# Kernel optimization log

Hardware: AMD Instinct MI355X
Metric: run time of the kernel (lower is better)

Reference implementation:

```python
import jax, jax.numpy as jnp
import numpy as np

NEG_SLOPE = 0.2  # PyG GATv2Conv default


def gatv2_layer(h, src, dst, Wl, bl, Wr, br, att, bias, n):
    # h: [N, din]; src/dst: [E'] (self-loops included)
    xl = h @ Wl + bl                      # [N, d] source-side transform (lin_l)
    xr = h @ Wr + br                      # [N, d] target-side transform (lin_r)
    s = xl[src] + xr[dst]                 # [E', d] per-edge gather
    e = jax.nn.leaky_relu(s, NEG_SLOPE) @ att  # [E'] GATv2 score
    # segment softmax over incoming edges of each dst node
    m = jax.ops.segment_max(e, dst, num_segments=n)
    ex = jnp.exp(e - m[dst])
    denom = jax.ops.segment_sum(ex, dst, num_segments=n)
    alpha = ex / denom[dst]               # [E']
    out = jax.ops.segment_sum(alpha[:, None] * xl[src], dst, num_segments=n)
    return out + bias                     # [N, d]


def setup_inputs() -> dict:
    key = jax.random.key(0)
    ks = jax.random.split(key, 9)
    n, e, d, L = 50000, 800000, 64, 3
    x = jax.random.normal(ks[0], (n, d), dtype=jnp.float32)
    edge_index = jax.random.randint(ks[1], (2, e), 0, n, dtype=jnp.int64)
    sc = 1.0 / np.sqrt(d)
    Wl = jax.random.normal(ks[2], (L, d, d), dtype=jnp.float32) * sc
    bl = jnp.zeros((L, d), dtype=jnp.float32)
    Wr = jax.random.normal(ks[3], (L, d, d), dtype=jnp.float32) * sc
    br = jnp.zeros((L, d), dtype=jnp.float32)
    att = jax.random.normal(ks[4], (L, d), dtype=jnp.float32) * sc
    bias = jnp.zeros((L, d), dtype=jnp.float32)
    return {"x": x, "edge_index": edge_index, "Wl": Wl, "bl": bl,
            "Wr": Wr, "br": br, "att": att, "bias": bias}


def reference(x, edge_index, Wl, bl, Wr, br, att, bias):
    n = x.shape[0]
    # PyG GATv2Conv default add_self_loops=True
    loops = jnp.arange(n, dtype=edge_index.dtype)
    src = jnp.concatenate([edge_index[0], loops])
    dst = jnp.concatenate([edge_index[1], loops])
    h = x
    num_layers = Wl.shape[0]
    for i in range(num_layers):
        h_new = jax.nn.relu(
            gatv2_layer(h, src, dst, Wl[i], bl[i], Wr[i], br[i], att[i], bias[i], n))
        # residual: applies at layer 0 too since in_dim == hidden_dim
        h = h_new + h
    return h
```

## Files before the change

kernel.cpp:

```cpp
#include <hip/hip_runtime.h>
#include <hip/hip_bf16.h>
#include <cmath>


#define D 64
#define CB 10
#define NBLK 512


__global__ __launch_bounds__(256) void hist_coarse_kernel(
    const int* __restrict__ ei, int* __restrict__ ghist, int E, int N, int NC) {
  __shared__ int h[64];
  int tid = threadIdx.x, blk = blockIdx.x;
  if (tid < 64) h[tid] = 0;
  __syncthreads();
  for (int eid = blk * 256 + tid; eid < E + N; eid += NBLK * 256) {
    int d = (eid < E) ? ei[E + eid] : (eid - E);
    atomicAdd(&h[d >> CB], 1);
  }
  __syncthreads();
  if (tid < NC) ghist[tid * NBLK + blk] = h[tid];
}

__global__ __launch_bounds__(1024) void scan_coarse_kernel(
    int* __restrict__ g, int* __restrict__ cbase, int M, int NC, int EP) {
  int tid = threadIdx.x;
  int chunk = (M + 1023) / 1024;
  int beg = tid * chunk;
  int end = min(M, beg + chunk);
  int sum = 0;
  for (int i = beg; i < end; ++i) sum += g[i];
  int lane = tid & 63, w = tid >> 6;
  int v = sum;
#pragma unroll
  for (int o = 1; o < 64; o <<= 1) {
    int t = __shfl_up(v, o, 64);
    if (lane >= o) v += t;
  }
  __shared__ int wsum[16], woff[16];
  if (lane == 63) wsum[w] = v;
  __syncthreads();
  if (tid == 0) { int r = 0; for (int i = 0; i < 16; ++i) { woff[i] = r; r += wsum[i]; } }
  __syncthreads();
  int run = woff[w] + (v - sum);
  for (int i = beg; i < end; ++i) {
    int old = g[i];
    g[i] = run;
    if ((i & (NBLK - 1)) == 0) cbase[i / NBLK] = run;
    run += old;
  }
  if (tid == 0) cbase[NC] = EP;
}

__global__ __launch_bounds__(256) void scatter_coarse_kernel(
    const int* __restrict__ ei, const int* __restrict__ g,
    unsigned* __restrict__ rec, int E, int N, int NC) {
  __shared__ int cur[64];
  int tid = threadIdx.x, blk = blockIdx.x;
  if (tid < NC) cur[tid] = g[tid * NBLK + blk];
  __syncthreads();
  for (int eid = blk * 256 + tid; eid < E + N; eid += NBLK * 256) {
    int s, d;
    if (eid < E) { s = ei[eid]; d = ei[E + eid]; }
    else         { s = d = eid - E; }
    int pos = atomicAdd(&cur[d >> CB], 1);
    rec[pos] = ((unsigned)(d & ((1 << CB) - 1)) << 16) | (unsigned)s;
  }
}

__global__ __launch_bounds__(1024) void buildcsr2_kernel(
    const unsigned* __restrict__ rec, const int* __restrict__ cbase,
    int* __restrict__ rowptr, unsigned short* __restrict__ csr_src,
    int N, int EP) {
  int c = blockIdx.x, tid = threadIdx.x;
  int bb = cbase[c], be = cbase[c + 1];
  __shared__ int hist[1024], cur[1024];
  hist[tid] = 0;
  __syncthreads();
  for (int p = bb + tid; p < be; p += 1024)
    atomicAdd(&hist[rec[p] >> 16], 1);
  __syncthreads();
  int dv = hist[tid];
  int lane = tid & 63, w = tid >> 6;
  int inc = dv;
#pragma unroll
  for (int o = 1; o < 64; o <<= 1) {
    int t = __shfl_up(inc, o, 64);
    if (lane >= o) inc += t;
  }
  __shared__ int wsum[16], woff[16];
  if (lane == 63) wsum[w] = inc;
  __syncthreads();
  if (tid == 0) { int r = 0; for (int i = 0; i < 16; ++i) { woff[i] = r; r += wsum[i]; } }
  __syncthreads();
  int excl = woff[w] + inc - dv;
  cur[tid] = excl;
  int node = (c << CB) + tid;
  if (node < N) rowptr[node] = bb + excl;
  if (c == 0 && tid == 0) rowptr[N] = EP;
  __syncthreads();
  for (int p = bb + tid; p < be; p += 1024) {
    unsigned r = rec[p];
    int pos = bb + atomicAdd(&cur[r >> 16], 1);
    csr_src[pos] = (unsigned short)(r & 0xFFFFu);
  }
}


__device__ __forceinline__ unsigned short f2bf(float f) {
  unsigned u = __float_as_uint(f);
  return (unsigned short)((u + 0x7FFFu + ((u >> 16) & 1u)) >> 16);
}
__device__ __forceinline__ float bflo(unsigned u) { return __uint_as_float(u << 16); }
__device__ __forceinline__ float bfhi(unsigned u) { return __uint_as_float(u & 0xFFFF0000u); }

__global__ __launch_bounds__(256) void transform_kernel(
    const float* __restrict__ h,
    const float* __restrict__ Wl, const float* __restrict__ bl,
    const float* __restrict__ Wr, const float* __restrict__ br,
    unsigned short* __restrict__ xlh, unsigned short* __restrict__ xrh, int N) {
  __shared__ float hs[16][D];
  int tid = threadIdx.x;
  int j = tid & 63;
  float wl[D], wr[D];
#pragma unroll
  for (int k = 0; k < D; ++k) {
    wl[k] = Wl[k * D + j];
    wr[k] = Wr[k * D + j];
  }
  int node0 = blockIdx.x * 16;
  for (int i = tid; i < 16 * D; i += 256) {
    int n = node0 + (i >> 6);
    hs[i >> 6][i & 63] = (n < N) ? h[(size_t)n * D + (i & 63)] : 0.f;
  }
  __syncthreads();
  float blj = bl[j], brj = br[j];
  int nl = tid >> 6;
  for (int g = 0; g < 4; ++g) {
    int local = nl * 4 + g;
    int n = node0 + local;
    float al = blj, ar = brj;
#pragma unroll
    for (int k4 = 0; k4 < D / 4; ++k4) {
      float4 hv = *reinterpret_cast<const float4*>(&hs[local][k4 * 4]);
      al = fmaf(hv.x, wl[k4 * 4 + 0], al);
      ar = fmaf(hv.x, wr[k4 * 4 + 0], ar);
      al = fmaf(hv.y, wl[k4 * 4 + 1], al);
      ar = fmaf(hv.y, wr[k4 * 4 + 1], ar);
      al = fmaf(hv.z, wl[k4 * 4 + 2], al);
      ar = fmaf(hv.z, wr[k4 * 4 + 2], ar);
      al = fmaf(hv.w, wl[k4 * 4 + 3], al);
      ar = fmaf(hv.w, wr[k4 * 4 + 3], ar);
    }
    if (n < N) {
      xlh[(size_t)n * D + j] = f2bf(al);
      xrh[(size_t)n * D + j] = f2bf(ar);
    }
  }
}


__global__ __launch_bounds__(256) void edge_kernel(
    const unsigned short* __restrict__ xlh, const unsigned short* __restrict__ xrh,
    const float* __restrict__ h_in, const int* __restrict__ rowptr,
    const unsigned short* __restrict__ csr_src, const float* __restrict__ att,
    const float* __restrict__ bias, float* __restrict__ h_out, int N) {
  int wv = (blockIdx.x * blockDim.x + threadIdx.x) >> 6;
  int lane = threadIdx.x & 63;
  int g = lane >> 4, l16 = lane & 15;
  int v = wv * 4 + g;
  if (v >= N) return;
  uint2 xq = *reinterpret_cast<const uint2*>(&xrh[(size_t)v * D + l16 * 4]);
  float4 xr4;
  xr4.x = bflo(xq.x); xr4.y = bfhi(xq.x);
  xr4.z = bflo(xq.y); xr4.w = bfhi(xq.y);
  float4 at4 = *reinterpret_cast<const float4*>(&att[l16 * 4]);
  int beg = rowptr[v], end = rowptr[v + 1];
  int deg = end - beg;
  int glane0 = g << 4;
  float m = -INFINITY, s = 0.f;
  float ax = 0.f, ay = 0.f, az = 0.f, aw = 0.f;
  int us = csr_src[min(beg + l16, end - 1)];
  for (int sc = 0; sc < deg; sc += 16) {
    int us_cur = us;
    if (sc + 16 < deg)
      us = csr_src[min(beg + sc + 16 + l16, end - 1)];
    int nt = min(16, deg - sc);
    for (int cc = 0; cc < nt; cc += 4) {
      float4 xu[4];
      float p[4];
#pragma unroll
      for (int k = 0; k < 4; ++k) {
        int u = __shfl(us_cur, glane0 + cc + k, 64);
        uint2 q = *reinterpret_cast<const uint2*>(&xlh[(size_t)u * D + l16 * 4]);
        xu[k].x = bflo(q.x);
        xu[k].y = bfhi(q.x);
        xu[k].z = bflo(q.y);
        xu[k].w = bfhi(q.y);
        float tx = xu[k].x + xr4.x, ty = xu[k].y + xr4.y;
        float tz = xu[k].z + xr4.z, tw = xu[k].w + xr4.w;
        tx = fmaxf(tx, 0.2f * tx);
        ty = fmaxf(ty, 0.2f * ty);
        tz = fmaxf(tz, 0.2f * tz);
        tw = fmaxf(tw, 0.2f * tw);
        float pp = tx * at4.x;
        pp = fmaf(ty, at4.y, pp);
        pp = fmaf(tz, at4.z, pp);
        pp = fmaf(tw, at4.w, pp);
        pp += __shfl_xor(pp, 1, 64);
        pp += __shfl_xor(pp, 2, 64);
        pp += __shfl_xor(pp, 4, 64);
        pp += __shfl_xor(pp, 8, 64);
        p[k] = (cc + k < nt) ? pp : -INFINITY;
      }
      float pm = fmaxf(fmaxf(p[0], p[1]), fmaxf(p[2], p[3]));
      float mn = fmaxf(m, pm);
      float a  = __expf(m - mn);
      float w0 = __expf(p[0] - mn);
      float w1 = __expf(p[1] - mn);
      float w2 = __expf(p[2] - mn);
      float w3 = __expf(p[3] - mn);
      s = s * a + (w0 + w1) + (w2 + w3);
      ax = fmaf(w0, xu[0].x, fmaf(w1, xu[1].x, fmaf(w2, xu[2].x, fmaf(w3, xu[3].x, ax * a))));
      ay = fmaf(w0, xu[0].y, fmaf(w1, xu[1].y, fmaf(w2, xu[2].y, fmaf(w3, xu[3].y, ay * a))));
      az = fmaf(w0, xu[0].z, fmaf(w1, xu[1].z, fmaf(w2, xu[2].z, fmaf(w3, xu[3].z, az * a))));
      aw = fmaf(w0, xu[0].w, fmaf(w1, xu[1].w, fmaf(w2, xu[2].w, fmaf(w3, xu[3].w, aw * a))));
      m = mn;
    }
  }
  float inv = 1.f / s;
  float4 b4v = *reinterpret_cast<const float4*>(&bias[l16 * 4]);
  float4 hv  = *reinterpret_cast<const float4*>(&h_in[(size_t)v * D + l16 * 4]);
  float4 o;
  o.x = fmaxf(ax * inv + b4v.x, 0.f) + hv.x;
  o.y = fmaxf(ay * inv + b4v.y, 0.f) + hv.y;
  o.z = fmaxf(az * inv + b4v.z, 0.f) + hv.z;
  o.w = fmaxf(aw * inv + b4v.w, 0.f) + hv.w;
  *reinterpret_cast<float4*>(&h_out[(size_t)v * D + l16 * 4]) = o;
}


extern "C" void kernel_launch(void* const* d_in, const int* in_sizes, int n_in,
                              void* d_out, int out_size, void* d_ws, size_t ws_size,
                              hipStream_t stream) {
  const float* x    = (const float*)d_in[0];
  const int*   ei   = (const int*)d_in[1];
  const float* Wl   = (const float*)d_in[2];
  const float* bl   = (const float*)d_in[3];
  const float* Wr   = (const float*)d_in[4];
  const float* br   = (const float*)d_in[5];
  const float* att  = (const float*)d_in[6];
  const float* bias = (const float*)d_in[7];

  int N = in_sizes[0] / D;
  int E = in_sizes[1] / 2;
  int L = in_sizes[2] / (D * D);
  int EP = E + N;
  int NC = (N + (1 << CB) - 1) >> CB;
  int M = NC * NBLK;

  float* hA = (float*)d_ws;
  float* hB = hA + (size_t)N * D;
  unsigned short* xlh = (unsigned short*)(hB + (size_t)N * D);
  unsigned short* xrh = xlh + (size_t)N * D;
  unsigned* rec = (unsigned*)(xrh + (size_t)N * D);
  unsigned short* csr_src = (unsigned short*)(rec + EP);
  int* rowptr   = (int*)(csr_src + ((EP + 1) & ~1));
  int* ghist    = rowptr + (N + 1);
  int* cbase    = ghist + M;

  hist_coarse_kernel<<<NBLK, 256, 0, stream>>>(ei, ghist, E, N, NC);
  scan_coarse_kernel<<<1, 1024, 0, stream>>>(ghist, cbase, M, NC, EP);
  scatter_coarse_kernel<<<NBLK, 256, 0, stream>>>(ei, ghist, rec, E, N, NC);
  buildcsr2_kernel<<<NC, 1024, 0, stream>>>(rec, cbase, rowptr, csr_src, N, EP);

  int nwaves = (N + 3) / 4;
  int nblocks = (nwaves * 64 + 255) / 256;
  const float* h_in = x;
  for (int l = 0; l < L; ++l) {
    float* h_out = (l == L - 1) ? (float*)d_out : ((l % 2 == 0) ? hA : hB);
    transform_kernel<<<(N + 15) / 16, 256, 0, stream>>>(
        h_in, Wl + (size_t)l * D * D, bl + (size_t)l * D,
        Wr + (size_t)l * D * D, br + (size_t)l * D, xlh, xrh, N);
    edge_kernel<<<nblocks, 256, 0, stream>>>(
        xlh, xrh, h_in, rowptr, csr_src, att + (size_t)l * D,
        bias + (size_t)l * D, h_out, N);
    h_in = h_out;
  }
}
```

Baseline: 218.6 us.

## Sort nodes by degree for balanced edge waves, lazy softmax rescale, persistent transform

Builds a degree histogram during CSR construction and counting-sorts nodes into a permutation by in-degree, so the four nodes sharing each edge-kernel wave have similar degree and less lane divergence. The online softmax now rescales its accumulators only when the running max rises by more than 8, which skips most exp and multiply work per chunk. The transform kernel becomes a grid-stride loop over 512 blocks, so the per-thread weight registers are loaded once per block instead of once per 16 nodes, and h is loaded as float4. The cost is two extra small kernels, an indirect perm lookup that scatters the node accesses, and less rescaling precision if scores overflow.

Result: faster. 205.8 us (-5.8%).

```diff
diff --git a/kernel.cpp b/kernel.cpp
--- a/kernel.cpp
+++ b/kernel.cpp
@@ -23,8 +23,10 @@
 }
 
 __global__ __launch_bounds__(1024) void scan_coarse_kernel(
-    int* __restrict__ g, int* __restrict__ cbase, int M, int NC, int EP) {
+    int* __restrict__ g, int* __restrict__ cbase, int* __restrict__ dh,
+    int M, int NC, int EP) {
   int tid = threadIdx.x;
+  if (tid < 64) dh[tid] = 0;
   int chunk = (M + 1023) / 1024;
   int beg = tid * chunk;
   int end = min(M, beg + chunk);
@@ -71,11 +73,13 @@
 __global__ __launch_bounds__(1024) void buildcsr2_kernel(
     const unsigned* __restrict__ rec, const int* __restrict__ cbase,
     int* __restrict__ rowptr, unsigned short* __restrict__ csr_src,
-    int N, int EP) {
+    int* __restrict__ dh, int N, int EP) {
   int c = blockIdx.x, tid = threadIdx.x;
   int bb = cbase[c], be = cbase[c + 1];
   __shared__ int hist[1024], cur[1024];
+  __shared__ int dloc[64];
   hist[tid] = 0;
+  if (tid < 64) dloc[tid] = 0;
   __syncthreads();
   for (int p = bb + tid; p < be; p += 1024)
     atomicAdd(&hist[rec[p] >> 16], 1);
@@ -96,9 +100,13 @@
   int excl = woff[w] + inc - dv;
   cur[tid] = excl;
   int node = (c << CB) + tid;
-  if (node < N) rowptr[node] = bb + excl;
+  if (node < N) {
+    rowptr[node] = bb + excl;
+    atomicAdd(&dloc[min(dv, 63)], 1);
+  }
   if (c == 0 && tid == 0) rowptr[N] = EP;
   __syncthreads();
+  if (tid < 64 && dloc[tid]) atomicAdd(&dh[tid], dloc[tid]);
   for (int p = bb + tid; p < be; p += 1024) {
     unsigned r = rec[p];
     int pos = bb + atomicAdd(&cur[r >> 16], 1);
@@ -106,6 +114,43 @@
   }
 }
 
+__global__ __launch_bounds__(64) void deg_scan_kernel(
+    const int* __restrict__ dh, int* __restrict__ dcur) {
+  int tid = threadIdx.x;
+  int v = dh[tid];
+  int orig = v;
+#pragma unroll
+  for (int o = 1; o < 64; o <<= 1) {
+    int t = __shfl_up(v, o, 64);
+    if (tid >= o) v += t;
+  }
+  dcur[tid] = v - orig;
+}
+
+__global__ __launch_bounds__(256) void deg_scatter_kernel(
+    const int* __restrict__ rowptr, int* __restrict__ dcur,
+    int* __restrict__ perm, int N) {
+  __shared__ int cnt[64], base[64], cur2[64];
+  int tid = threadIdx.x;
+  if (tid < 64) { cnt[tid] = 0; cur2[tid] = 0; }
+  __syncthreads();
+  int i = blockIdx.x * 256 + tid;
+  int bin = 0;
+  bool act = (i < N);
+  if (act) {
+    int deg = rowptr[i + 1] - rowptr[i];
+    bin = min(deg, 63);
+    atomicAdd(&cnt[bin], 1);
+  }
+  __syncthreads();
+  if (tid < 64 && cnt[tid]) base[tid] = atomicAdd(&dcur[tid], cnt[tid]);
+  __syncthreads();
+  if (act) {
+    int pos = base[bin] + atomicAdd(&cur2[bin], 1);
+    perm[pos] = i;
+  }
+}
+
 
 __device__ __forceinline__ unsigned short f2bf(float f) {
   unsigned u = __float_as_uint(f);
@@ -118,7 +163,8 @@
     const float* __restrict__ h,
     const float* __restrict__ Wl, const float* __restrict__ bl,
     const float* __restrict__ Wr, const float* __restrict__ br,
-    unsigned short* __restrict__ xlh, unsigned short* __restrict__ xrh, int N) {
+    unsigned short* __restrict__ xlh, unsigned short* __restrict__ xrh,
+    int N, int ntiles) {
   __shared__ float hs[16][D];
   int tid = threadIdx.x;
   int j = tid & 63;
@@ -128,33 +174,37 @@
     wl[k] = Wl[k * D + j];
     wr[k] = Wr[k * D + j];
   }
-  int node0 = blockIdx.x * 16;
-  for (int i = tid; i < 16 * D; i += 256) {
-    int n = node0 + (i >> 6);
-    hs[i >> 6][i & 63] = (n < N) ? h[(size_t)n * D + (i & 63)] : 0.f;
-  }
-  __syncthreads();
   float blj = bl[j], brj = br[j];
   int nl = tid >> 6;
-  for (int g = 0; g < 4; ++g) {
-    int local = nl * 4 + g;
-    int n = node0 + local;
-    float al = blj, ar = brj;
-#pragma unroll
-    for (int k4 = 0; k4 < D / 4; ++k4) {
-      float4 hv = *reinterpret_cast<const float4*>(&hs[local][k4 * 4]);
-      al = fmaf(hv.x, wl[k4 * 4 + 0], al);
-      ar = fmaf(hv.x, wr[k4 * 4 + 0], ar);
-      al = fmaf(hv.y, wl[k4 * 4 + 1], al);
-      ar = fmaf(hv.y, wr[k4 * 4 + 1], ar);
-      al = fmaf(hv.z, wl[k4 * 4 + 2], al);
-      ar = fmaf(hv.z, wr[k4 * 4 + 2], ar);
-      al = fmaf(hv.w, wl[k4 * 4 + 3], al);
-      ar = fmaf(hv.w, wr[k4 * 4 + 3], ar);
-    }
-    if (n < N) {
-      xlh[(size_t)n * D + j] = f2bf(al);
-      xrh[(size_t)n * D + j] = f2bf(ar);
+  int lr = tid >> 4, lc = (tid & 15) * 4;
+  for (int tile = blockIdx.x; tile < ntiles; tile += gridDim.x) {
+    int node0 = tile * 16;
+    __syncthreads();
+    int n = node0 + lr;
+    float4 hv4 = make_float4(0.f, 0.f, 0.f, 0.f);
+    if (n < N) hv4 = *reinterpret_cast<const float4*>(&h[(size_t)n * D + lc]);
+    *reinterpret_cast<float4*>(&hs[lr][lc]) = hv4;
+    __syncthreads();
+    for (int g = 0; g < 4; ++g) {
+      int local = nl * 4 + g;
+      int nn = node0 + local;
+      float al = blj, ar = brj;
+#pragma unroll
+      for (int k4 = 0; k4 < D / 4; ++k4) {
+        float4 hv = *reinterpret_cast<const float4*>(&hs[local][k4 * 4]);
+        al = fmaf(hv.x, wl[k4 * 4 + 0], al);
+        ar = fmaf(hv.x, wr[k4 * 4 + 0], ar);
+        al = fmaf(hv.y, wl[k4 * 4 + 1], al);
+        ar = fmaf(hv.y, wr[k4 * 4 + 1], ar);
+        al = fmaf(hv.z, wl[k4 * 4 + 2], al);
+        ar = fmaf(hv.z, wr[k4 * 4 + 2], ar);
+        al = fmaf(hv.w, wl[k4 * 4 + 3], al);
+        ar = fmaf(hv.w, wr[k4 * 4 + 3], ar);
+      }
+      if (nn < N) {
+        xlh[(size_t)nn * D + j] = f2bf(al);
+        xrh[(size_t)nn * D + j] = f2bf(ar);
+      }
     }
   }
 }
@@ -163,13 +213,15 @@
 __global__ __launch_bounds__(256) void edge_kernel(
     const unsigned short* __restrict__ xlh, const unsigned short* __restrict__ xrh,
     const float* __restrict__ h_in, const int* __restrict__ rowptr,
-    const unsigned short* __restrict__ csr_src, const float* __restrict__ att,
-    const float* __restrict__ bias, float* __restrict__ h_out, int N) {
+    const unsigned short* __restrict__ csr_src, const int* __restrict__ perm,
+    const float* __restrict__ att, const float* __restrict__ bias,
+    float* __restrict__ h_out, int N) {
   int wv = (blockIdx.x * blockDim.x + threadIdx.x) >> 6;
   int lane = threadIdx.x & 63;
   int g = lane >> 4, l16 = lane & 15;
-  int v = wv * 4 + g;
-  if (v >= N) return;
+  int idx = wv * 4 + g;
+  if (idx >= N) return;
+  int v = perm[idx];
   uint2 xq = *reinterpret_cast<const uint2*>(&xrh[(size_t)v * D + l16 * 4]);
   float4 xr4;
   xr4.x = bflo(xq.x); xr4.y = bfhi(xq.x);
@@ -214,18 +266,20 @@
         p[k] = (cc + k < nt) ? pp : -INFINITY;
       }
       float pm = fmaxf(fmaxf(p[0], p[1]), fmaxf(p[2], p[3]));
-      float mn = fmaxf(m, pm);
-      float a  = __expf(m - mn);
-      float w0 = __expf(p[0] - mn);
-      float w1 = __expf(p[1] - mn);
-      float w2 = __expf(p[2] - mn);
-      float w3 = __expf(p[3] - mn);
-      s = s * a + (w0 + w1) + (w2 + w3);
-      ax = fmaf(w0, xu[0].x, fmaf(w1, xu[1].x, fmaf(w2, xu[2].x, fmaf(w3, xu[3].x, ax * a))));
-      ay = fmaf(w0, xu[0].y, fmaf(w1, xu[1].y, fmaf(w2, xu[2].y, fmaf(w3, xu[3].y, ay * a))));
-      az = fmaf(w0, xu[0].z, fmaf(w1, xu[1].z, fmaf(w2, xu[2].z, fmaf(w3, xu[3].z, az * a))));
-      aw = fmaf(w0, xu[0].w, fmaf(w1, xu[1].w, fmaf(w2, xu[2].w, fmaf(w3, xu[3].w, aw * a))));
-      m = mn;
+      if (pm > m + 8.0f) {
+        float a = __expf(m - pm);
+        s *= a; ax *= a; ay *= a; az *= a; aw *= a;
+        m = pm;
+      }
+      float w0 = __expf(p[0] - m);
+      float w1 = __expf(p[1] - m);
+      float w2 = __expf(p[2] - m);
+      float w3 = __expf(p[3] - m);
+      s += (w0 + w1) + (w2 + w3);
+      ax = fmaf(w0, xu[0].x, fmaf(w1, xu[1].x, fmaf(w2, xu[2].x, fmaf(w3, xu[3].x, ax))));
+      ay = fmaf(w0, xu[0].y, fmaf(w1, xu[1].y, fmaf(w2, xu[2].y, fmaf(w3, xu[3].y, ay))));
+      az = fmaf(w0, xu[0].z, fmaf(w1, xu[1].z, fmaf(w2, xu[2].z, fmaf(w3, xu[3].z, az))));
+      aw = fmaf(w0, xu[0].w, fmaf(w1, xu[1].w, fmaf(w2, xu[2].w, fmaf(w3, xu[3].w, aw))));
     }
   }
   float inv = 1.f / s;
@@ -268,22 +322,28 @@
   int* rowptr   = (int*)(csr_src + ((EP + 1) & ~1));
   int* ghist    = rowptr + (N + 1);
   int* cbase    = ghist + M;
+  int* dh       = cbase + (NC + 1);
+  int* dcur     = dh + 64;
+  int* perm     = dcur + 64;
 
   hist_coarse_kernel<<<NBLK, 256, 0, stream>>>(ei, ghist, E, N, NC);
-  scan_coarse_kernel<<<1, 1024, 0, stream>>>(ghist, cbase, M, NC, EP);
+  scan_coarse_kernel<<<1, 1024, 0, stream>>>(ghist, cbase, dh, M, NC, EP);
   scatter_coarse_kernel<<<NBLK, 256, 0, stream>>>(ei, ghist, rec, E, N, NC);
-  buildcsr2_kernel<<<NC, 1024, 0, stream>>>(rec, cbase, rowptr, csr_src, N, EP);
-
+  buildcsr2_kernel<<<NC, 1024, 0, stream>>>(rec, cbase, rowptr, csr_src, dh, N, EP);
+  deg_scan_kernel<<<1, 64, 0, stream>>>(dh, dcur);
+  deg_scatter_kernel<<<(N + 255) / 256, 256, 0, stream>>>(rowptr, dcur, perm, N);
+
+  int ntiles = (N + 15) / 16;
   int nwaves = (N + 3) / 4;
   int nblocks = (nwaves * 64 + 255) / 256;
   const float* h_in = x;
   for (int l = 0; l < L; ++l) {
     float* h_out = (l == L - 1) ? (float*)d_out : ((l % 2 == 0) ? hA : hB);
-    transform_kernel<<<(N + 15) / 16, 256, 0, stream>>>(
+    transform_kernel<<<512, 256, 0, stream>>>(
         h_in, Wl + (size_t)l * D * D, bl + (size_t)l * D,
-        Wr + (size_t)l * D * D, br + (size_t)l * D, xlh, xrh, N);
+        Wr + (size_t)l * D * D, br + (size_t)l * D, xlh, xrh, N, ntiles);
     edge_kernel<<<nblocks, 256, 0, stream>>>(
-        xlh, xrh, h_in, rowptr, csr_src, att + (size_t)l * D,
+        xlh, xrh, h_in, rowptr, csr_src, perm, att + (size_t)l * D,
         bias + (size_t)l * D, h_out, N);
     h_in = h_out;
   }
```
